# Optimization experiments

Measured on AMD Instinct MI355X. Metric: run time of the kernel, lower is better.

The kernel has to match this reference:

```python
import jax, jax.numpy as jnp
import numpy as np

B, S, H, NH = 2, 2048, 1024, 16
DH = H // NH  # 64

def setup_inputs() -> dict:
    key = jax.random.key(0)
    ks = jax.random.split(key, 6)
    return {
        "hidden_states": jax.random.normal(ks[0], (B, S, H), jnp.float32),
        "attention_mask": jnp.zeros((B, 1, 1, S), jnp.float32),  # additive mask (0 = attend)
        "local_attention_mask": jax.random.randint(ks[1], (B, 1, S, S), 0, 2).astype(jnp.int32),
        "gate_outputs": jax.random.uniform(ks[2], (B, NH, S, 1), jnp.float32),
        "Wq": jax.random.normal(ks[3], (H, H), jnp.float32) * 0.02,
        "bq": jnp.zeros((H,), jnp.float32),
        "Wk": jax.random.normal(ks[4], (H, H), jnp.float32) * 0.02,
        "bk": jnp.zeros((H,), jnp.float32),
        "Wv": jax.random.normal(ks[5], (H, H), jnp.float32) * 0.02,
        "bv": jnp.zeros((H,), jnp.float32),
    }

def _heads(x):
    # [B,S,H] -> [B,NH,S,DH]
    return x.reshape(B, S, NH, DH).transpose(0, 2, 1, 3)

def reference(hidden_states, attention_mask, local_attention_mask, gate_outputs, Wq, bq, Wk, bk, Wv, bv):
    q = _heads(hidden_states @ Wq.T + bq)
    k = _heads(hidden_states @ Wk.T + bk)
    v = _heads(hidden_states @ Wv.T + bv)
    scores = jnp.einsum("bhqd,bhkd->bhqk", q, k) / jnp.sqrt(jnp.float32(DH))
    # global branch (additive mask)
    probs_g = jax.nn.softmax(scores + attention_mask, axis=-1)
    ctx_g = jnp.einsum("bhqk,bhkd->bhqd", probs_g, v)
    # local branch: 0/1 mask -> additive -inf mask
    lmask = (1.0 - local_attention_mask.astype(jnp.float32)) * jnp.finfo(jnp.float32).min
    probs_l = jax.nn.softmax(scores + lmask, axis=-1)
    ctx_l = jnp.einsum("bhqk,bhkd->bhqd", probs_l, v)
    ctx = gate_outputs * ctx_l + (1.0 - gate_outputs) * ctx_g  # [B,NH,S,DH]
    return ctx.transpose(0, 2, 1, 3).reshape(B, S, H)
```

## Files before the change

kernel.cpp:

```cpp
#include <hip/hip_runtime.h>
#include <cstdint>
#include <cstddef>

typedef short short8 __attribute__((ext_vector_type(8)));
typedef short short4v __attribute__((ext_vector_type(4)));
typedef float floatx4 __attribute__((ext_vector_type(4)));
typedef unsigned short ushort4v __attribute__((ext_vector_type(4)));
typedef unsigned int uintx4 __attribute__((ext_vector_type(4)));

constexpr int B_ = 2, S_ = 2048, H_ = 1024, NH_ = 16, DH_ = 64;
constexpr int K_ = H_;

__device__ __forceinline__ unsigned short f2bf(float f) {
  unsigned u = __float_as_uint(f);
  u += 0x7fffu + ((u >> 16) & 1u);
  return (unsigned short)(u >> 16);
}

__device__ __forceinline__ unsigned cvtpk(float a, float b) {
  unsigned r;
  asm("v_cvt_pk_bf16_f32 %0, %1, %2" : "=v"(r) : "v"(a), "v"(b));
  return r;
}

__global__ __launch_bounds__(256) void prep_kernel(
    const float* __restrict__ hs, unsigned short* __restrict__ hbf,
    const float* __restrict__ Wq, const float* __restrict__ Wk, const float* __restrict__ Wv,
    unsigned short* __restrict__ wqb, unsigned short* __restrict__ wkb,
    unsigned short* __restrict__ wvb,
    const int* __restrict__ lm, unsigned long long* __restrict__ bm,
    const float* __restrict__ am, float* __restrict__ ea) {
  const int bid = blockIdx.x, tid = threadIdx.x;
  if (bid < 7168) {
    const float* in;
    unsigned short* out;
    int off;
    if (bid < 4096) { in = hs; out = hbf; off = bid; }
    else {
      int wsel = (bid - 4096) >> 10;
      in = (wsel == 0) ? Wq : (wsel == 1) ? Wk : Wv;
      out = (wsel == 0) ? wqb : (wsel == 1) ? wkb : wvb;
      off = (bid - 4096) & 1023;
    }
    int i = (off * 256 + tid) * 4;
    float4 v = *reinterpret_cast<const float4*>(in + i);
    ushort4v o;
    o.x = f2bf(v.x); o.y = f2bf(v.y); o.z = f2bf(v.z); o.w = f2bf(v.w);
    *reinterpret_cast<ushort4v*>(out + i) = o;
  } else if (bid < 39936) {
    int word = (bid - 7168) * 4 + (tid >> 6);
    int lane = tid & 63;
    unsigned long long bits = __ballot(lm[(size_t)word * 64 + lane] != 0);
    if (lane == 0) bm[word] = bits;
  } else {
    int i = (bid - 39936) * 256 + tid;
    ea[i] = __expf(am[i]);
  }
}

typedef __attribute__((address_space(1))) const void gvoid;
typedef __attribute__((address_space(3))) void lvoid;
__device__ __forceinline__ void async16(const unsigned short* gp, unsigned short* lp) {
  __builtin_amdgcn_global_load_lds((gvoid*)gp, (lvoid*)lp, 16, 0, 0);
}

__global__ __launch_bounds__(256) void gemm_qkv(
    const unsigned short* __restrict__ A,
    const unsigned short* __restrict__ Wq, const unsigned short* __restrict__ Wk,
    const unsigned short* __restrict__ Wv,
    const float* __restrict__ bq, const float* __restrict__ bk, const float* __restrict__ bv,
    unsigned short* __restrict__ qo, unsigned short* __restrict__ ko,
    unsigned short* __restrict__ vo) {
  __shared__ alignas(16) unsigned short As[128 * 32];
  __shared__ alignas(16) unsigned short Bs[128 * 32];
  const int z = blockIdx.z;
  const unsigned short* W = (z == 0) ? Wq : (z == 1) ? Wk : Wv;
  const float* bias = (z == 0) ? bq : (z == 1) ? bk : bv;

  const int m0 = blockIdx.x * 128, n0 = blockIdx.y * 128;
  const int tid = threadIdx.x, lane = tid & 63, wvi = tid >> 6;
  const int wr = wvi >> 1, wc = wvi & 1, quad = lane >> 4, l16 = lane & 15;

  floatx4 zf = {0.f, 0.f, 0.f, 0.f};
  floatx4 acc[4][4];
  for (int i = 0; i < 4; i++)
    for (int j = 0; j < 4; j++) acc[i][j] = zf;

  for (int kk = 0; kk < K_; kk += 32) {
#pragma unroll
    for (int i = 0; i < 2; i++) {
      int cb = wvi * 128 + i * 64;
      int c = cb + lane;
      int row = c >> 2, kc = c & 3;
      async16(A + (size_t)(m0 + row) * K_ + kk + kc * 8, As + cb * 8);
      async16(W + (size_t)(n0 + row) * K_ + kk + kc * 8, Bs + cb * 8);
    }
    __syncthreads();
    short8 af[4], bfr[4];
#pragma unroll
    for (int mf = 0; mf < 4; mf++)
      af[mf] = *reinterpret_cast<const short8*>(&As[(wr * 64 + mf * 16 + l16) * 32 + quad * 8]);
#pragma unroll
    for (int nf = 0; nf < 4; nf++)
      bfr[nf] = *reinterpret_cast<const short8*>(&Bs[(wc * 64 + nf * 16 + l16) * 32 + quad * 8]);
    if (z == 2) {
#pragma unroll
      for (int mf = 0; mf < 4; mf++)
#pragma unroll
        for (int nf = 0; nf < 4; nf++)
          acc[mf][nf] = __builtin_amdgcn_mfma_f32_16x16x32_bf16(af[mf], bfr[nf], acc[mf][nf], 0, 0, 0);
    } else {
#pragma unroll
      for (int mf = 0; mf < 4; mf++)
#pragma unroll
        for (int nf = 0; nf < 4; nf++)
          acc[mf][nf] = __builtin_amdgcn_mfma_f32_16x16x32_bf16(bfr[nf], af[mf], acc[mf][nf], 0, 0, 0);
    }
    __syncthreads();
  }

  if (z == 2) {
#pragma unroll
    for (int mf = 0; mf < 4; mf++) {
      int mbase = m0 + wr * 64 + mf * 16 + quad * 4;
      int b = mbase >> 11, s0 = mbase & 2047;
      int kl = s0 & 63;
#pragma unroll
      for (int nf = 0; nf < 4; nf++) {
        int n = n0 + wc * 64 + nf * 16 + l16;
        int h = n >> 6, d = n & 63;
        int bh = b * NH_ + h;
        float bvv = bias[n];
        floatx4 c = acc[mf][nf];
        size_t base = (size_t)bh * 131072 + (s0 >> 6) * 4096 + (d >> 4) * 1024 +
                      (kl >> 5) * 512 + ((kl >> 3) & 3) * 128 + (d & 15) * 8 + (kl & 7);
        ushort4v p;
        p.x = f2bf(c[0] + bvv); p.y = f2bf(c[1] + bvv);
        p.z = f2bf(c[2] + bvv); p.w = f2bf(c[3] + bvv);
        *reinterpret_cast<ushort4v*>(&vo[base]) = p;
      }
    }
  } else {
#pragma unroll
    for (int mf = 0; mf < 4; mf++) {
      int s = m0 + wr * 64 + mf * 16 + l16;
      int b = s >> 11;
      int sq = s & 2047;
#pragma unroll
      for (int nf = 0; nf < 4; nf++) {
        int nn = n0 + wc * 64 + nf * 16 + quad * 4;
        int h = nn >> 6, dh = nn & 63;
        int bh = b * NH_ + h;
        float4 b4 = *reinterpret_cast<const float4*>(bias + nn);
        floatx4 c = acc[mf][nf];
        if (z == 0) {
          ushort4v p;
          p.x = f2bf((c[0] + b4.x) * 0.18033688011112042f);
          p.y = f2bf((c[1] + b4.y) * 0.18033688011112042f);
          p.z = f2bf((c[2] + b4.z) * 0.18033688011112042f);
          p.w = f2bf((c[3] + b4.w) * 0.18033688011112042f);
          *reinterpret_cast<ushort4v*>(&qo[((size_t)bh * S_ + sq) * DH_ + dh]) = p;
        } else {
          int kl = sq & 63;
          int t = ((kl >> 4) & 2) | ((kl >> 2) & 1);
          int rr = ((kl >> 1) & 12) | (kl & 3);
          size_t base = (size_t)bh * 131072 + (sq >> 6) * 4096 + t * 1024 +
                        (dh >> 5) * 512 + ((dh >> 3) & 3) * 128 + rr * 8 + (dh & 7);
          ushort4v p;
          p.x = f2bf(c[0] + b4.x); p.y = f2bf(c[1] + b4.y);
          p.z = f2bf(c[2] + b4.z); p.w = f2bf(c[3] + b4.w);
          *reinterpret_cast<ushort4v*>(&ko[base]) = p;
        }
      }
    }
  }
}

__global__ __launch_bounds__(256, 4) void attn_kernel(
    const unsigned short* __restrict__ q,
    const unsigned short* __restrict__ kperm,
    const unsigned short* __restrict__ vperm,
    const float* __restrict__ eam,
    const unsigned long long* __restrict__ bm,
    const float* __restrict__ gate,
    float* __restrict__ out) {
  __shared__ alignas(16) unsigned short Ks[2][4096];
  __shared__ alignas(16) unsigned short Vs[2][4096];

  const int flat = blockIdx.x;
  const int h = (flat & 7) + 8 * ((flat >> 3) & 1);
  const int b = (flat >> 4) & 1;
  const int qt = flat >> 5;
  const int tid = threadIdx.x, lane = tid & 63, wvi = tid >> 6;
  const int quad = lane >> 4, l16 = lane & 15;
  const int bh = b * NH_ + h;
  const int q0 = qt * 64 + wvi * 16;
  const int quad8 = quad * 8;

  const unsigned short* qrow = q + ((size_t)bh * S_ + q0 + l16) * DH_;
  short8 qf0 = *reinterpret_cast<const short8*>(qrow + quad * 8);
  short8 qf1 = *reinterpret_cast<const short8*>(qrow + 32 + quad * 8);

  floatx4 zf = {0.f, 0.f, 0.f, 0.f};
  float psg = 0.f, psl = 0.f;
  floatx4 accg[4], accl[4];
#pragma unroll
  for (int i = 0; i < 4; i++) { accg[i] = zf; accl[i] = zf; }

  const unsigned short* kp = kperm + (size_t)bh * 131072;
  const unsigned short* vp = vperm + (size_t)bh * 131072;
  const float* eamb = eam + (size_t)b * S_;
  const unsigned long long* bmq = bm + ((size_t)b * S_ + q0 + l16) * (S_ / 64);

  const int soA = tid * 8, soB = 2048 + tid * 8;
  const unsigned short* kgA = kp + soA;
  const unsigned short* kgB = kp + soB;
  const unsigned short* vgA = vp + soA;
  const unsigned short* vgB = vp + soB;

  uint4 pk0 = *reinterpret_cast<const uint4*>(kgA);
  uint4 pk1 = *reinterpret_cast<const uint4*>(kgB);
  uint4 pv0 = *reinterpret_cast<const uint4*>(vgA);
  uint4 pv1 = *reinterpret_cast<const uint4*>(vgB);
  *reinterpret_cast<uint4*>(&Ks[0][soA]) = pk0;
  *reinterpret_cast<uint4*>(&Ks[0][soB]) = pk1;
  *reinterpret_cast<uint4*>(&Vs[0][soA]) = pv0;
  *reinterpret_cast<uint4*>(&Vs[0][soB]) = pv1;
  pk0 = *reinterpret_cast<const uint4*>(kgA + 4096);
  pk1 = *reinterpret_cast<const uint4*>(kgB + 4096);
  pv0 = *reinterpret_cast<const uint4*>(vgA + 4096);
  pv1 = *reinterpret_cast<const uint4*>(vgB + 4096);

  for (int kt = 0; kt < S_ / 64; kt++) {
    __syncthreads();
    {
      const int bn = (kt + 1) & 1;
      *reinterpret_cast<uint4*>(&Ks[bn][soA]) = pk0;
      *reinterpret_cast<uint4*>(&Ks[bn][soB]) = pk1;
      *reinterpret_cast<uint4*>(&Vs[bn][soA]) = pv0;
      *reinterpret_cast<uint4*>(&Vs[bn][soB]) = pv1;
    }
    {
      const int tb = ((kt + 2) & 31) * 4096;
      pk0 = *reinterpret_cast<const uint4*>(kgA + tb);
      pk1 = *reinterpret_cast<const uint4*>(kgB + tb);
      pv0 = *reinterpret_cast<const uint4*>(vgA + tb);
      pv1 = *reinterpret_cast<const uint4*>(vgB + tb);
    }
    const int k0 = kt * 64;
    uint2 wv = *reinterpret_cast<const uint2*>(&bmq[kt]);
    unsigned wq0 = wv.x >> quad8;
    unsigned wq1 = wv.y >> quad8;
    float4 ea0 = *reinterpret_cast<const float4*>(eamb + k0 + quad8);
    float4 ea1 = *reinterpret_cast<const float4*>(eamb + k0 + 4 + quad8);
    float4 ea2 = *reinterpret_cast<const float4*>(eamb + k0 + 32 + quad8);
    float4 ea3 = *reinterpret_cast<const float4*>(eamb + k0 + 36 + quad8);

    const unsigned short* Kc = Ks[kt & 1];
    const unsigned short* Vc = Vs[kt & 1];
    floatx4 scT[4];
#pragma unroll
    for (int t = 0; t < 4; t++) {
      const unsigned short* kr = Kc + t * 1024 + lane * 8;
      short8 kf0 = *reinterpret_cast<const short8*>(kr);
      short8 kf1 = *reinterpret_cast<const short8*>(kr + 512);
      scT[t] = __builtin_amdgcn_mfma_f32_16x16x32_bf16(kf0, qf0, zf, 0, 0, 0);
      scT[t] = __builtin_amdgcn_mfma_f32_16x16x32_bf16(kf1, qf1, scT[t], 0, 0, 0);
    }
    uintx4 fgv[2], flv[2];
#pragma unroll
    for (int t = 0; t < 4; t++) {
      const int T = t >> 1, tau = t & 1;
      floatx4 sc = scT[t];
      unsigned wq = T ? wq1 : wq0;
      float4 ea = (t == 0) ? ea0 : (t == 1) ? ea1 : (t == 2) ? ea2 : ea3;
      unsigned m4 = (wq >> (tau * 4)) & 0xFu;
      float e0 = __builtin_amdgcn_exp2f(sc[0]);
      float e1 = __builtin_amdgcn_exp2f(sc[1]);
      float e2 = __builtin_amdgcn_exp2f(sc[2]);
      float e3 = __builtin_amdgcn_exp2f(sc[3]);
      float g0 = e0 * ea.x, g1 = e1 * ea.y, g2 = e2 * ea.z, g3 = e3 * ea.w;
      psg += (g0 + g1) + (g2 + g3);
      float l0 = (m4 & 1u) ? e0 : 0.f;
      float l1 = (m4 & 2u) ? e1 : 0.f;
      float l2 = (m4 & 4u) ? e2 : 0.f;
      float l3 = (m4 & 8u) ? e3 : 0.f;
      psl += (l0 + l1) + (l2 + l3);
      fgv[T][tau * 2]     = cvtpk(g0, g1);
      fgv[T][tau * 2 + 1] = cvtpk(g2, g3);
      flv[T][tau * 2]     = cvtpk(l0, l1);
      flv[T][tau * 2 + 1] = cvtpk(l2, l3);
    }
    short8 FG0 = __builtin_bit_cast(short8, fgv[0]);
    short8 FG1 = __builtin_bit_cast(short8, fgv[1]);
    short8 FL0 = __builtin_bit_cast(short8, flv[0]);
    short8 FL1 = __builtin_bit_cast(short8, flv[1]);
#pragma unroll
    for (int d = 0; d < 4; d++) {
      const unsigned short* vb = Vc + d * 1024 + lane * 8;
      short8 v0 = *reinterpret_cast<const short8*>(vb);
      short8 v1 = *reinterpret_cast<const short8*>(vb + 512);
      accg[d] = __builtin_amdgcn_mfma_f32_16x16x32_bf16(v0, FG0, accg[d], 0, 0, 0);
      accl[d] = __builtin_amdgcn_mfma_f32_16x16x32_bf16(v0, FL0, accl[d], 0, 0, 0);
      accg[d] = __builtin_amdgcn_mfma_f32_16x16x32_bf16(v1, FG1, accg[d], 0, 0, 0);
      accl[d] = __builtin_amdgcn_mfma_f32_16x16x32_bf16(v1, FL1, accl[d], 0, 0, 0);
    }
  }

  float lgf = psg;
  lgf += __shfl_xor(lgf, 16, 64);
  lgf += __shfl_xor(lgf, 32, 64);
  float llf = psl;
  llf += __shfl_xor(llf, 16, 64);
  llf += __shfl_xor(llf, 32, 64);
  const int s = q0 + l16;
  const float g = gate[(size_t)bh * S_ + s];
  const float cg = (1.f - g) / lgf, cl = g / llf;
  float* orow = out + ((size_t)b * S_ + s) * H_ + h * DH_ + quad * 4;
#pragma unroll
  for (int d = 0; d < 4; d++) {
    float4 o;
    o.x = cl * accl[d][0] + cg * accg[d][0];
    o.y = cl * accl[d][1] + cg * accg[d][1];
    o.z = cl * accl[d][2] + cg * accg[d][2];
    o.w = cl * accl[d][3] + cg * accg[d][3];
    *reinterpret_cast<float4*>(orow + d * 16) = o;
  }
}

extern "C" void kernel_launch(void* const* d_in, const int* in_sizes, int n_in,
                              void* d_out, int out_size, void* d_ws, size_t ws_size,
                              hipStream_t stream) {
  (void)in_sizes; (void)n_in; (void)out_size; (void)ws_size;
  const float* hs = (const float*)d_in[0];
  const float* am = (const float*)d_in[1];
  const int* lm = (const int*)d_in[2];
  const float* gate = (const float*)d_in[3];
  const float* Wq = (const float*)d_in[4];
  const float* bq = (const float*)d_in[5];
  const float* Wk = (const float*)d_in[6];
  const float* bk = (const float*)d_in[7];
  const float* Wv = (const float*)d_in[8];
  const float* bv = (const float*)d_in[9];
  float* out = (float*)d_out;

  unsigned short* ws = (unsigned short*)d_ws;
  unsigned short* hbf = ws;
  unsigned short* wqb = hbf + 4194304;
  unsigned short* wkb = wqb + 1048576;
  unsigned short* wvb = wkb + 1048576;
  unsigned short* qb = wvb + 1048576;
  unsigned short* kb = qb + 4194304;
  unsigned short* vtb = kb + 4194304;
  unsigned long long* bmp = (unsigned long long*)(vtb + 4194304);
  float* eamp = (float*)(bmp + 131072);

  prep_kernel<<<39952, 256, 0, stream>>>(hs, hbf, Wq, Wk, Wv, wqb, wkb, wvb, lm, bmp, am, eamp);
  gemm_qkv<<<dim3(32, 8, 3), 256, 0, stream>>>(hbf, wqb, wkb, wvb, bq, bk, bv, qb, kb, vtb);
  attn_kernel<<<dim3(1024), 256, 0, stream>>>(qb, kb, vtb, eamp, bmp, gate, out);
}
```

Before: 229.8 us.

## Use async global-to-LDS loads, MFMA row-sum denominators, and MFMA priority hints

Replaces the register-staged K/V double buffering with async 16-byte global-to-LDS copies issued one tile ahead, which frees VGPRs and removes the explicit LDS store instructions. Softmax denominators are now computed by extra MFMAs against a ones vector instead of scalar VALU adds followed by cross-lane shuffles. The MFMA sections are also wrapped in s_setprio raises. In exchange the kernel runs four more MFMAs per tile, and the denominators are accumulated from bf16-rounded probabilities, which changes numerics slightly.

```diff
diff --git a/kernel.cpp b/kernel.cpp
--- a/kernel.cpp
+++ b/kernel.cpp
@@ -3,7 +3,6 @@
 #include <cstddef>
 
 typedef short short8 __attribute__((ext_vector_type(8)));
-typedef short short4v __attribute__((ext_vector_type(4)));
 typedef float floatx4 __attribute__((ext_vector_type(4)));
 typedef unsigned short ushort4v __attribute__((ext_vector_type(4)));
 typedef unsigned int uintx4 __attribute__((ext_vector_type(4)));
@@ -202,63 +201,54 @@
   short8 qf1 = *reinterpret_cast<const short8*>(qrow + 32 + quad * 8);
 
   floatx4 zf = {0.f, 0.f, 0.f, 0.f};
-  float psg = 0.f, psl = 0.f;
   floatx4 accg[4], accl[4];
+  floatx4 deng = zf, denl = zf;
 #pragma unroll
   for (int i = 0; i < 4; i++) { accg[i] = zf; accl[i] = zf; }
+
+  const short8 onesf = {(short)0x3F80, (short)0x3F80, (short)0x3F80, (short)0x3F80,
+                        (short)0x3F80, (short)0x3F80, (short)0x3F80, (short)0x3F80};
 
   const unsigned short* kp = kperm + (size_t)bh * 131072;
   const unsigned short* vp = vperm + (size_t)bh * 131072;
   const float* eamb = eam + (size_t)b * S_;
   const unsigned long long* bmq = bm + ((size_t)b * S_ + q0 + l16) * (S_ / 64);
 
-  const int soA = tid * 8, soB = 2048 + tid * 8;
-  const unsigned short* kgA = kp + soA;
-  const unsigned short* kgB = kp + soB;
-  const unsigned short* vgA = vp + soA;
-  const unsigned short* vgB = vp + soB;
-
-  uint4 pk0 = *reinterpret_cast<const uint4*>(kgA);
-  uint4 pk1 = *reinterpret_cast<const uint4*>(kgB);
-  uint4 pv0 = *reinterpret_cast<const uint4*>(vgA);
-  uint4 pv1 = *reinterpret_cast<const uint4*>(vgB);
-  *reinterpret_cast<uint4*>(&Ks[0][soA]) = pk0;
-  *reinterpret_cast<uint4*>(&Ks[0][soB]) = pk1;
-  *reinterpret_cast<uint4*>(&Vs[0][soA]) = pv0;
-  *reinterpret_cast<uint4*>(&Vs[0][soB]) = pv1;
-  pk0 = *reinterpret_cast<const uint4*>(kgA + 4096);
-  pk1 = *reinterpret_cast<const uint4*>(kgB + 4096);
-  pv0 = *reinterpret_cast<const uint4*>(vgA + 4096);
-  pv1 = *reinterpret_cast<const uint4*>(vgB + 4096);
+  const int tid8 = tid * 8;
+  const unsigned short* kgA = kp + tid8;
+  const unsigned short* kgB = kp + 2048 + tid8;
+  const unsigned short* vgA = vp + tid8;
+  const unsigned short* vgB = vp + 2048 + tid8;
+  const int wb = wvi * 512;
+
+  async16(kgA, &Ks[0][wb]);
+  async16(kgB, &Ks[0][2048 + wb]);
+  async16(vgA, &Vs[0][wb]);
+  async16(vgB, &Vs[0][2048 + wb]);
 
   for (int kt = 0; kt < S_ / 64; kt++) {
     __syncthreads();
-    {
-      const int bn = (kt + 1) & 1;
-      *reinterpret_cast<uint4*>(&Ks[bn][soA]) = pk0;
-      *reinterpret_cast<uint4*>(&Ks[bn][soB]) = pk1;
-      *reinterpret_cast<uint4*>(&Vs[bn][soA]) = pv0;
-      *reinterpret_cast<uint4*>(&Vs[bn][soB]) = pv1;
-    }
-    {
-      const int tb = ((kt + 2) & 31) * 4096;
-      pk0 = *reinterpret_cast<const uint4*>(kgA + tb);
-      pk1 = *reinterpret_cast<const uint4*>(kgB + tb);
-      pv0 = *reinterpret_cast<const uint4*>(vgA + tb);
-      pv1 = *reinterpret_cast<const uint4*>(vgB + tb);
-    }
     const int k0 = kt * 64;
     uint2 wv = *reinterpret_cast<const uint2*>(&bmq[kt]);
-    unsigned wq0 = wv.x >> quad8;
-    unsigned wq1 = wv.y >> quad8;
     float4 ea0 = *reinterpret_cast<const float4*>(eamb + k0 + quad8);
     float4 ea1 = *reinterpret_cast<const float4*>(eamb + k0 + 4 + quad8);
     float4 ea2 = *reinterpret_cast<const float4*>(eamb + k0 + 32 + quad8);
     float4 ea3 = *reinterpret_cast<const float4*>(eamb + k0 + 36 + quad8);
+    unsigned wq0 = wv.x >> quad8;
+    unsigned wq1 = wv.y >> quad8;
+    if (kt != S_ / 64 - 1) {
+      const int bn = (kt + 1) & 1;
+      const size_t tb = (size_t)(kt + 1) * 4096;
+      async16(kgA + tb, &Ks[bn][wb]);
+      async16(kgB + tb, &Ks[bn][2048 + wb]);
+      async16(vgA + tb, &Vs[bn][wb]);
+      async16(vgB + tb, &Vs[bn][2048 + wb]);
+    }
 
     const unsigned short* Kc = Ks[kt & 1];
     const unsigned short* Vc = Vs[kt & 1];
     floatx4 scT[4];
+    __builtin_amdgcn_s_setprio(1);
 #pragma unroll
     for (int t = 0; t < 4; t++) {
       const unsigned short* kr = Kc + t * 1024 + lane * 8;
@@ -267,6 +257,7 @@
       scT[t] = __builtin_amdgcn_mfma_f32_16x16x32_bf16(kf0, qf0, zf, 0, 0, 0);
       scT[t] = __builtin_amdgcn_mfma_f32_16x16x32_bf16(kf1, qf1, scT[t], 0, 0, 0);
     }
+    __builtin_amdgcn_s_setprio(0);
     uintx4 fgv[2], flv[2];
 #pragma unroll
     for (int t = 0; t < 4; t++) {
@@ -280,12 +271,10 @@
       float e2 = __builtin_amdgcn_exp2f(sc[2]);
       float e3 = __builtin_amdgcn_exp2f(sc[3]);
       float g0 = e0 * ea.x, g1 = e1 * ea.y, g2 = e2 * ea.z, g3 = e3 * ea.w;
-      psg += (g0 + g1) + (g2 + g3);
       float l0 = (m4 & 1u) ? e0 : 0.f;
       float l1 = (m4 & 2u) ? e1 : 0.f;
       float l2 = (m4 & 4u) ? e2 : 0.f;
       float l3 = (m4 & 8u) ? e3 : 0.f;
-      psl += (l0 + l1) + (l2 + l3);
       fgv[T][tau * 2]     = cvtpk(g0, g1);
       fgv[T][tau * 2 + 1] = cvtpk(g2, g3);
       flv[T][tau * 2]     = cvtpk(l0, l1);
@@ -295,6 +284,11 @@
     short8 FG1 = __builtin_bit_cast(short8, fgv[1]);
     short8 FL0 = __builtin_bit_cast(short8, flv[0]);
     short8 FL1 = __builtin_bit_cast(short8, flv[1]);
+    __builtin_amdgcn_s_setprio(1);
+    deng = __builtin_amdgcn_mfma_f32_16x16x32_bf16(onesf, FG0, deng, 0, 0, 0);
+    denl = __builtin_amdgcn_mfma_f32_16x16x32_bf16(onesf, FL0, denl, 0, 0, 0);
+    deng = __builtin_amdgcn_mfma_f32_16x16x32_bf16(onesf, FG1, deng, 0, 0, 0);
+    denl = __builtin_amdgcn_mfma_f32_16x16x32_bf16(onesf, FL1, denl, 0, 0, 0);
 #pragma unroll
     for (int d = 0; d < 4; d++) {
       const unsigned short* vb = Vc + d * 1024 + lane * 8;
@@ -305,14 +299,11 @@
       accg[d] = __builtin_amdgcn_mfma_f32_16x16x32_bf16(v1, FG1, accg[d], 0, 0, 0);
       accl[d] = __builtin_amdgcn_mfma_f32_16x16x32_bf16(v1, FL1, accl[d], 0, 0, 0);
     }
-  }
-
-  float lgf = psg;
-  lgf += __shfl_xor(lgf, 16, 64);
-  lgf += __shfl_xor(lgf, 32, 64);
-  float llf = psl;
-  llf += __shfl_xor(llf, 16, 64);
-  llf += __shfl_xor(llf, 32, 64);
+    __builtin_amdgcn_s_setprio(0);
+  }
+
+  const float lgf = deng[0];
+  const float llf = denl[0];
   const int s = q0 + l16;
   const float g = gate[(size_t)bh * S_ + s];
   const float cg = (1.f - g) / lgf, cl = g / llf;
```

New measurement: 231.2 us. Within noise of the previous version (+0.6%).
